# Kernel optimization log

Hardware: AMD Instinct MI355X
Metric: run time of the kernel (lower is better)

Reference implementation:

```python
import jax, jax.numpy as jnp
import numpy as np

B = 262144
I = 128  # input_size
H = 128  # hidden_size


def setup_inputs() -> dict:
    key = jax.random.key(0)
    ks = jax.random.split(key, 12)
    std = 1.0 / np.sqrt(H)
    u = lambda k, shape: jax.random.uniform(k, shape, jnp.float32, -std, std)
    return {
        "inputs": jax.random.normal(ks[0], (B, I), jnp.float32),
        "h_prev": jax.random.normal(ks[1], (B, H), jnp.float32),
        "c_prev": jax.random.normal(ks[2], (B, H), jnp.float32),
        "W_ii": u(ks[3], (H, I)), "W_hi": u(ks[4], (H, H)),
        "W_if": u(ks[5], (H, I)), "W_hf": u(ks[6], (H, H)),
        "W_io": u(ks[7], (H, I)), "W_ho": u(ks[8], (H, H)),
        "W_ig": u(ks[9], (H, I)), "W_hg": u(ks[10], (H, H)),
    }


def reference(inputs, h_prev, c_prev, W_ii, W_hi, W_if, W_hf, W_io, W_ho, W_ig, W_hg):
    # Same math as 8 separate GEMMs, expressed as 2 fused GEMMs over concatenated gates.
    W_x = jnp.concatenate([W_ii, W_if, W_io, W_ig], axis=0)  # [4H, I]
    W_h = jnp.concatenate([W_hi, W_hf, W_ho, W_hg], axis=0)  # [4H, H]
    gates = inputs @ W_x.T + h_prev @ W_h.T  # [B, 4H]
    gi, gf, go, gg = jnp.split(gates, 4, axis=-1)
    i_t = jax.nn.sigmoid(gi)
    f_t = jax.nn.sigmoid(gf)
    o_t = jax.nn.sigmoid(go)
    g_t = jnp.tanh(gg)
    c_t = f_t * c_prev + i_t * g_t
    h_t = o_t * jnp.tanh(c_t)
    return jnp.stack([h_t, c_t], axis=0)  # [2, B, H]
```

## Files before the change

### kernel.cpp

```cpp
#include <hip/hip_runtime.h>

#define BATCH 262144
#define NBLK 512
#define NITER 32
#define ROWS 32
#define ASTRIDE 264
#define GSTRIDE 68
#define GPLANE (ROWS * GSTRIDE)
#define BH 33554432

typedef __attribute__((ext_vector_type(8))) short bf16x8;
typedef __attribute__((ext_vector_type(4))) float f32x4;
typedef __attribute__((ext_vector_type(8))) unsigned short u16x8;

__device__ __forceinline__ unsigned short f2bf(float f) {
  unsigned int u = __float_as_uint(f);
  u += 0x7fffu + ((u >> 16) & 1u);
  return (unsigned short)(u >> 16);
}

__device__ __forceinline__ float fexp(float x) { return __builtin_amdgcn_exp2f(x * 1.44269504f); }
__device__ __forceinline__ float sigm(float x) { return __builtin_amdgcn_rcpf(1.f + fexp(-x)); }
__device__ __forceinline__ float ftanh(float x) { return 1.f - 2.f * __builtin_amdgcn_rcpf(1.f + fexp(2.f * x)); }

__global__ __launch_bounds__(512, 4) void lstm_fused(
    const float* __restrict__ X, const float* __restrict__ H0, const float* __restrict__ C0,
    const float* __restrict__ Wii, const float* __restrict__ Whi,
    const float* __restrict__ Wif, const float* __restrict__ Whf,
    const float* __restrict__ Wio, const float* __restrict__ Who,
    const float* __restrict__ Wig, const float* __restrict__ Whg,
    float* __restrict__ Out) {
  __shared__ __align__(16) unsigned short Abuf[2][ROWS * ASTRIDE];
  __shared__ __align__(16) float Glds[4 * GPLANE];

  const int tid = threadIdx.x;
  const int wave = tid >> 6;
  const int lane = tid & 63;
  const int lrow = lane & 15;
  const int lkq = lane >> 4;
  const int ct = wave & 3;
  const int gp = wave >> 2;

  const int bid = blockIdx.x;
  const int xcd = bid & 7;
  const int ch = (bid >> 3) & 1;
  const int p = bid >> 4;
  const int tbase = p + 32 * xcd;
  const int col0 = ch * 64;

  const int hcol = col0 + ct * 16 + lrow;

  const float* Wxp[4] = {Wii, Wif, Wio, Wig};
  const float* Whp[4] = {Whi, Whf, Who, Whg};

  bf16x8 wf[2][8];
#pragma unroll
  for (int gg = 0; gg < 2; ++gg) {
    const int g = gp * 2 + gg;
#pragma unroll
    for (int kk = 0; kk < 8; ++kk) {
      const int k = kk * 32 + lkq * 8;
      const float* src = (kk < 4) ? (Wxp[g] + hcol * 128 + k)
                                  : (Whp[g] + hcol * 128 + (k - 128));
      float4 lo = *(const float4*)src;
      float4 hi = *(const float4*)(src + 4);
      bf16x8 w;
      w[0] = (short)f2bf(lo.x); w[1] = (short)f2bf(lo.y);
      w[2] = (short)f2bf(lo.z); w[3] = (short)f2bf(lo.w);
      w[4] = (short)f2bf(hi.x); w[5] = (short)f2bf(hi.y);
      w[6] = (short)f2bf(hi.z); w[7] = (short)f2bf(hi.w);
      wf[gg][kk] = w;
    }
  }

  const int r0 = tid >> 4;
  const int ci = tid & 15;
  float4 s0, s1, s2, s3;
  float cva[4];

#define ISSUE_LOADS(ROW0) do {                                            \
    const float* b_ = (ci < 8)                                            \
        ? (X + (size_t)((ROW0) + r0) * 128 + ci * 16)                     \
        : (H0 + (size_t)((ROW0) + r0) * 128 + (ci - 8) * 16);             \
    s0 = ((const float4*)b_)[0];  s1 = ((const float4*)b_)[1];            \
    s2 = ((const float4*)b_)[2];  s3 = ((const float4*)b_)[3];            \
  } while (0)

#define ISSUE_CV(ROW0) do {                                               \
    _Pragma("unroll")                                                     \
    for (int j_ = 0; j_ < 4; ++j_)                                        \
      cva[j_] = C0[(size_t)((ROW0) + 4 * wave + j_) * 128 + col0 + lane]; \
  } while (0)

#define CVT8(DST, A, B) do {                                              \
    u16x8 t_;                                                             \
    t_[0] = f2bf((A).x); t_[1] = f2bf((A).y);                             \
    t_[2] = f2bf((A).z); t_[3] = f2bf((A).w);                             \
    t_[4] = f2bf((B).x); t_[5] = f2bf((B).y);                             \
    t_[6] = f2bf((B).z); t_[7] = f2bf((B).w);                             \
    *(u16x8*)(DST) = t_;                                                  \
  } while (0)

#define BODY(IT, AB) do {                                                 \
    const int row0_ = (tbase + (IT) * 256) * ROWS;                        \
                                             \
    CVT8(&(AB)[r0 * ASTRIDE + ci * 16], s0, s1);                          \
    CVT8(&(AB)[r0 * ASTRIDE + ci * 16 + 8], s2, s3);                      \
    __syncthreads();    \
    ISSUE_CV(row0_);          \
                                  \
    f32x4 a00 = {0.f, 0.f, 0.f, 0.f}, a01 = a00, a10 = a00, a11 = a00;    \
    _Pragma("unroll")                                                     \
    for (int kk = 0; kk < 8; ++kk) {                                      \
      bf16x8 aA = *(const bf16x8*)&(AB)[lrow * ASTRIDE + kk * 32 + lkq * 8];        \
      bf16x8 aB = *(const bf16x8*)&(AB)[(16 + lrow) * ASTRIDE + kk * 32 + lkq * 8]; \
      a00 = __builtin_amdgcn_mfma_f32_16x16x32_bf16(aA, wf[0][kk], a00, 0, 0, 0);   \
      a01 = __builtin_amdgcn_mfma_f32_16x16x32_bf16(aA, wf[1][kk], a01, 0, 0, 0);   \
      a10 = __builtin_amdgcn_mfma_f32_16x16x32_bf16(aB, wf[0][kk], a10, 0, 0, 0);   \
      a11 = __builtin_amdgcn_mfma_f32_16x16x32_bf16(aB, wf[1][kk], a11, 0, 0, 0);   \
    }                                                                     \
                                          \
    _Pragma("unroll")                                                     \
    for (int j_ = 0; j_ < 4; ++j_) {                                      \
      const int gr = (lkq * 4 + j_) * GSTRIDE + ct * 16 + lrow;           \
      Glds[(gp * 2 + 0) * GPLANE + gr] = a00[j_];                         \
      Glds[(gp * 2 + 1) * GPLANE + gr] = a01[j_];                         \
      Glds[(gp * 2 + 0) * GPLANE + 16 * GSTRIDE + gr] = a10[j_];          \
      Glds[(gp * 2 + 1) * GPLANE + 16 * GSTRIDE + gr] = a11[j_];          \
    }                                                                     \
    __syncthreads();                         \
                \
    if ((IT) + 1 < NITER) ISSUE_LOADS(row0_ + 256 * ROWS);                \
      \
    _Pragma("unroll")                                                     \
    for (int j_ = 0; j_ < 4; ++j_) {                                      \
      const int rl = 4 * wave + j_;                                       \
      const float gi = Glds[0 * GPLANE + rl * GSTRIDE + lane];            \
      const float gf = Glds[1 * GPLANE + rl * GSTRIDE + lane];            \
      const float go = Glds[2 * GPLANE + rl * GSTRIDE + lane];            \
      const float gc = Glds[3 * GPLANE + rl * GSTRIDE + lane];            \
      const float itv = sigm(gi);                                         \
      const float ftv = sigm(gf);                                         \
      const float otv = sigm(go);                                         \
      const float gtv = ftanh(gc);                                        \
      const float ctv = ftv * cva[j_] + itv * gtv;                        \
      const float htv = otv * ftanh(ctv);                                 \
      const size_t o_ = (size_t)(row0_ + rl) * 128 + col0 + lane;         \
      Out[o_] = htv;                                                      \
      Out[BH + o_] = ctv;                                                 \
    }                                                                     \
  } while (0)

  ISSUE_LOADS(tbase * ROWS);

  for (int it = 0; it < NITER; it += 2) {
    BODY(it, &Abuf[0][0]);
    BODY(it + 1, &Abuf[1][0]);
  }

#undef ISSUE_LOADS
#undef ISSUE_CV
#undef CVT8
#undef BODY
}

extern "C" void kernel_launch(void* const* d_in, const int* in_sizes, int n_in,
                              void* d_out, int out_size, void* d_ws, size_t ws_size,
                              hipStream_t stream) {
  (void)in_sizes; (void)n_in; (void)out_size; (void)d_ws; (void)ws_size;
  lstm_fused<<<NBLK, 512, 0, stream>>>(
      (const float*)d_in[0], (const float*)d_in[1], (const float*)d_in[2],
      (const float*)d_in[3], (const float*)d_in[4], (const float*)d_in[5],
      (const float*)d_in[6], (const float*)d_in[7], (const float*)d_in[8],
      (const float*)d_in[9], (const float*)d_in[10],
      (float*)d_out);
}
```

Before: 178.8 us.

## Give each wave all four gates for its columns, drop LDS gate staging

Each wave now holds weights for all four gates of its 16 hidden columns, with the MFMA operands swapped so gate accumulators land in registers aligned with the output layout. This removes the LDS gate exchange buffer and its second block-wide barrier per iteration. Blocks shrink to 256 threads, so each thread loads twice as much input, and outputs and c_prev move as 16-byte nontemporal vector accesses. Register pressure rises (32 weight fragments per lane plus 16 accumulators) and there are fewer waves per block to hide memory latency.

```diff
diff --git a/kernel.cpp b/kernel.cpp
--- a/kernel.cpp
+++ b/kernel.cpp
@@ -5,8 +5,6 @@
 #define NITER 32
 #define ROWS 32
 #define ASTRIDE 264
-#define GSTRIDE 68
-#define GPLANE (ROWS * GSTRIDE)
 #define BH 33554432
 
 typedef __attribute__((ext_vector_type(8))) short bf16x8;
@@ -23,7 +21,7 @@
 __device__ __forceinline__ float sigm(float x) { return __builtin_amdgcn_rcpf(1.f + fexp(-x)); }
 __device__ __forceinline__ float ftanh(float x) { return 1.f - 2.f * __builtin_amdgcn_rcpf(1.f + fexp(2.f * x)); }
 
-__global__ __launch_bounds__(512, 4) void lstm_fused(
+__global__ __launch_bounds__(256, 2) void lstm_fused(
     const float* __restrict__ X, const float* __restrict__ H0, const float* __restrict__ C0,
     const float* __restrict__ Wii, const float* __restrict__ Whi,
     const float* __restrict__ Wif, const float* __restrict__ Whf,
@@ -31,32 +29,27 @@
     const float* __restrict__ Wig, const float* __restrict__ Whg,
     float* __restrict__ Out) {
   __shared__ __align__(16) unsigned short Abuf[2][ROWS * ASTRIDE];
-  __shared__ __align__(16) float Glds[4 * GPLANE];
 
   const int tid = threadIdx.x;
   const int wave = tid >> 6;
   const int lane = tid & 63;
   const int lrow = lane & 15;
   const int lkq = lane >> 4;
-  const int ct = wave & 3;
-  const int gp = wave >> 2;
 
   const int bid = blockIdx.x;
   const int xcd = bid & 7;
   const int ch = (bid >> 3) & 1;
   const int p = bid >> 4;
   const int tbase = p + 32 * xcd;
-  const int col0 = ch * 64;
-
-  const int hcol = col0 + ct * 16 + lrow;
+  const int colbase = ch * 64 + wave * 16;
+  const int hcol = colbase + lrow;
 
   const float* Wxp[4] = {Wii, Wif, Wio, Wig};
   const float* Whp[4] = {Whi, Whf, Who, Whg};
 
-  bf16x8 wf[2][8];
+  bf16x8 wf[4][8];
 #pragma unroll
-  for (int gg = 0; gg < 2; ++gg) {
-    const int g = gp * 2 + gg;
+  for (int g = 0; g < 4; ++g) {
 #pragma unroll
     for (int kk = 0; kk < 8; ++kk) {
       const int k = kk * 32 + lkq * 8;
@@ -69,27 +62,25 @@
       w[2] = (short)f2bf(lo.z); w[3] = (short)f2bf(lo.w);
       w[4] = (short)f2bf(hi.x); w[5] = (short)f2bf(hi.y);
       w[6] = (short)f2bf(hi.z); w[7] = (short)f2bf(hi.w);
-      wf[gg][kk] = w;
+      wf[g][kk] = w;
     }
   }
 
   const int r0 = tid >> 4;
   const int ci = tid & 15;
-  float4 s0, s1, s2, s3;
-  float cva[4];
+  const int coff = ci * 16;
+  float4 s0, s1, s2, s3, s4, s5, s6, s7;
+  f32x4 cv0, cv1;
 
 #define ISSUE_LOADS(ROW0) do {                                            \
-    const float* b_ = (ci < 8)                                            \
+    const float* pA_ = (ci < 8)                                           \
         ? (X + (size_t)((ROW0) + r0) * 128 + ci * 16)                     \
         : (H0 + (size_t)((ROW0) + r0) * 128 + (ci - 8) * 16);             \
-    s0 = ((const float4*)b_)[0];  s1 = ((const float4*)b_)[1];            \
-    s2 = ((const float4*)b_)[2];  s3 = ((const float4*)b_)[3];            \
-  } while (0)
-
-#define ISSUE_CV(ROW0) do {                                               \
-    _Pragma("unroll")                                                     \
-    for (int j_ = 0; j_ < 4; ++j_)                                        \
-      cva[j_] = C0[(size_t)((ROW0) + 4 * wave + j_) * 128 + col0 + lane]; \
+    s0 = ((const float4*)pA_)[0];  s1 = ((const float4*)pA_)[1];          \
+    s2 = ((const float4*)pA_)[2];  s3 = ((const float4*)pA_)[3];          \
+    const float* pB_ = pA_ + 16 * 128;                                    \
+    s4 = ((const float4*)pB_)[0];  s5 = ((const float4*)pB_)[1];          \
+    s6 = ((const float4*)pB_)[2];  s7 = ((const float4*)pB_)[3];          \
   } while (0)
 
 #define CVT8(DST, A, B) do {                                              \
@@ -101,54 +92,50 @@
     *(u16x8*)(DST) = t_;                                                  \
   } while (0)
 
+#define MT(MT_, CV, AB, ROW0) do {                                        \
+    f32x4 a0 = {0.f, 0.f, 0.f, 0.f}, a1 = a0, a2 = a0, a3 = a0;           \
+    _Pragma("unroll")                                                     \
+    for (int kk = 0; kk < 8; ++kk) {                                      \
+      bf16x8 b_ = *(const bf16x8*)&(AB)[((MT_)*16 + lrow) * ASTRIDE + kk * 32 + lkq * 8]; \
+      a0 = __builtin_amdgcn_mfma_f32_16x16x32_bf16(wf[0][kk], b_, a0, 0, 0, 0); \
+      a1 = __builtin_amdgcn_mfma_f32_16x16x32_bf16(wf[1][kk], b_, a1, 0, 0, 0); \
+      a2 = __builtin_amdgcn_mfma_f32_16x16x32_bf16(wf[2][kk], b_, a2, 0, 0, 0); \
+      a3 = __builtin_amdgcn_mfma_f32_16x16x32_bf16(wf[3][kk], b_, a3, 0, 0, 0); \
+    }                                                                     \
+    f32x4 hv_, cf_;                                                       \
+    _Pragma("unroll")                                                     \
+    for (int j = 0; j < 4; ++j) {                                         \
+      const float itv = sigm(a0[j]);                                      \
+      const float ftv = sigm(a1[j]);                                      \
+      const float otv = sigm(a2[j]);                                      \
+      const float gtv = ftanh(a3[j]);                                     \
+      const float ctv = ftv * (CV)[j] + itv * gtv;                        \
+      cf_[j] = ctv;                                                       \
+      hv_[j] = otv * ftanh(ctv);                                          \
+    }                                                                     \
+    const size_t ob_ = (size_t)((ROW0) + (MT_)*16 + lrow) * 128 + colbase + lkq * 4; \
+    __builtin_nontemporal_store(hv_, (f32x4*)(Out + ob_));                \
+    __builtin_nontemporal_store(cf_, (f32x4*)(Out + BH + ob_));           \
+  } while (0)
+
 #define BODY(IT, AB) do {                                                 \
     const int row0_ = (tbase + (IT) * 256) * ROWS;                        \
-                                             \
-    CVT8(&(AB)[r0 * ASTRIDE + ci * 16], s0, s1);                          \
-    CVT8(&(AB)[r0 * ASTRIDE + ci * 16 + 8], s2, s3);                      \
-    __syncthreads();    \
-    ISSUE_CV(row0_);          \
-                                  \
-    f32x4 a00 = {0.f, 0.f, 0.f, 0.f}, a01 = a00, a10 = a00, a11 = a00;    \
-    _Pragma("unroll")                                                     \
-    for (int kk = 0; kk < 8; ++kk) {                                      \
-      bf16x8 aA = *(const bf16x8*)&(AB)[lrow * ASTRIDE + kk * 32 + lkq * 8];        \
-      bf16x8 aB = *(const bf16x8*)&(AB)[(16 + lrow) * ASTRIDE + kk * 32 + lkq * 8]; \
-      a00 = __builtin_amdgcn_mfma_f32_16x16x32_bf16(aA, wf[0][kk], a00, 0, 0, 0);   \
-      a01 = __builtin_amdgcn_mfma_f32_16x16x32_bf16(aA, wf[1][kk], a01, 0, 0, 0);   \
-      a10 = __builtin_amdgcn_mfma_f32_16x16x32_bf16(aB, wf[0][kk], a10, 0, 0, 0);   \
-      a11 = __builtin_amdgcn_mfma_f32_16x16x32_bf16(aB, wf[1][kk], a11, 0, 0, 0);   \
-    }                                                                     \
-                                          \
-    _Pragma("unroll")                                                     \
-    for (int j_ = 0; j_ < 4; ++j_) {                                      \
-      const int gr = (lkq * 4 + j_) * GSTRIDE + ct * 16 + lrow;           \
-      Glds[(gp * 2 + 0) * GPLANE + gr] = a00[j_];                         \
-      Glds[(gp * 2 + 1) * GPLANE + gr] = a01[j_];                         \
-      Glds[(gp * 2 + 0) * GPLANE + 16 * GSTRIDE + gr] = a10[j_];          \
-      Glds[(gp * 2 + 1) * GPLANE + 16 * GSTRIDE + gr] = a11[j_];          \
-    }                                                                     \
-    __syncthreads();                         \
-                \
+                          \
+    CVT8(&(AB)[r0 * ASTRIDE + coff], s0, s1);                             \
+    CVT8(&(AB)[r0 * ASTRIDE + coff + 8], s2, s3);                         \
+    CVT8(&(AB)[(r0 + 16) * ASTRIDE + coff], s4, s5);                      \
+    CVT8(&(AB)[(r0 + 16) * ASTRIDE + coff + 8], s6, s7);                  \
+    __syncthreads();         \
+       \
+       \
+                                            \
+    cv0 = __builtin_nontemporal_load(                                     \
+        (const f32x4*)(C0 + (size_t)(row0_ + lrow) * 128 + colbase + lkq * 4));      \
+    cv1 = __builtin_nontemporal_load(                                     \
+        (const f32x4*)(C0 + (size_t)(row0_ + 16 + lrow) * 128 + colbase + lkq * 4)); \
     if ((IT) + 1 < NITER) ISSUE_LOADS(row0_ + 256 * ROWS);                \
-      \
-    _Pragma("unroll")                                                     \
-    for (int j_ = 0; j_ < 4; ++j_) {                                      \
-      const int rl = 4 * wave + j_;                                       \
-      const float gi = Glds[0 * GPLANE + rl * GSTRIDE + lane];            \
-      const float gf = Glds[1 * GPLANE + rl * GSTRIDE + lane];            \
-      const float go = Glds[2 * GPLANE + rl * GSTRIDE + lane];            \
-      const float gc = Glds[3 * GPLANE + rl * GSTRIDE + lane];            \
-      const float itv = sigm(gi);                                         \
-      const float ftv = sigm(gf);                                         \
-      const float otv = sigm(go);                                         \
-      const float gtv = ftanh(gc);                                        \
-      const float ctv = ftv * cva[j_] + itv * gtv;                        \
-      const float htv = otv * ftanh(ctv);                                 \
-      const size_t o_ = (size_t)(row0_ + rl) * 128 + col0 + lane;         \
-      Out[o_] = htv;                                                      \
-      Out[BH + o_] = ctv;                                                 \
-    }                                                                     \
+    MT(0, cv0, AB, row0_);                                                \
+    MT(1, cv1, AB, row0_);                                                \
   } while (0)
 
   ISSUE_LOADS(tbase * ROWS);
@@ -159,8 +146,8 @@
   }
 
 #undef ISSUE_LOADS
-#undef ISSUE_CV
 #undef CVT8
+#undef MT
 #undef BODY
 }
 
@@ -168,7 +155,7 @@
                               void* d_out, int out_size, void* d_ws, size_t ws_size,
                               hipStream_t stream) {
   (void)in_sizes; (void)n_in; (void)out_size; (void)d_ws; (void)ws_size;
-  lstm_fused<<<NBLK, 512, 0, stream>>>(
+  lstm_fused<<<NBLK, 256, 0, stream>>>(
       (const float*)d_in[0], (const float*)d_in[1], (const float*)d_in[2],
       (const float*)d_in[3], (const float*)d_in[4], (const float*)d_in[5],
       (const float*)d_in[6], (const float*)d_in[7], (const float*)d_in[8],
```

After: 166.5 us. 6.9% less time.
